# Kernel tuning notes

Hardware: AMD Instinct MI355X
Metric: run time of the kernel (lower is better)

Reference implementation:

```python
import jax, jax.numpy as jnp
import numpy as np

B, R, A, S, F, N = 2, 1, 16, 14, 1024, 512  # batch, num_rx, num_rx_ant, ofdm_symbols, fft_size, num_effective_sc
D = S * N  # flattened time-frequency dim that C acts on


def setup_inputs() -> dict:
    key = jax.random.key(0)
    k0, k1, k2, k3 = jax.random.split(key, 4)
    scale = 1.0 / np.sqrt(D).astype(np.float32)
    x_re = jax.random.normal(k0, (B, R, A, S, F), jnp.float32)
    x_im = jax.random.normal(k1, (B, R, A, S, F), jnp.float32)
    C_re = jax.random.normal(k2, (D, D), jnp.float32) * scale
    C_im = jax.random.normal(k3, (D, D), jnp.float32) * scale
    # unique, sorted effective-subcarrier indices (as in an OFDM ResourceGrid)
    sc_ind = jnp.asarray(np.sort(np.random.default_rng(0).choice(F, N, replace=False)), jnp.int32)
    return {"x_re": x_re, "x_im": x_im, "C_re": C_re, "C_im": C_im, "sc_ind": sc_ind}


def reference(x_re, x_im, C_re, C_im, sc_ind):
    x = jax.lax.complex(x_re, x_im)            # [B,R,A,S,F] complex64
    C = jax.lax.complex(C_re, C_im)            # [D,D]
    y = jnp.take(x, sc_ind, axis=-1)           # gather effective subcarriers -> [B,R,A,S,N]
    b, r, a, s, n = y.shape
    yf = y.reshape(b, r, a, s * n)             # flatten_last_dims(y, 2)
    # multiply_from_right with adjoint: yf @ C^H
    yf = jnp.einsum('brad,ed->brae', yf, jnp.conj(C))
    y = yf.reshape(b, r, a, s, n)
    # scatter back into full fft_size grid (unique indices -> set == scatter_nd on zeros)
    out = jnp.zeros((b, r, a, s, F), y.dtype).at[..., sc_ind].set(y)
    return jnp.stack([out.real, out.imag])     # [2,B,R,A,S,F] (real, imag)
```

## Files before the change

kernel.cpp:

```cpp
#include <hip/hip_runtime.h>
#include <hip/hip_bf16.h>

#define B_ 2
#define R_ 1
#define A_ 16
#define S_ 14
#define F_ 1024
#define N_ 512
#define D_ (S_*N_)
#define M_ (B_*R_*A_)
#define KK_ (2*D_)
#define BE 64
#define ETILES (D_/BE)

typedef __attribute__((ext_vector_type(8))) short bf16x8;
typedef __attribute__((ext_vector_type(4))) float f32x4;

static __device__ inline short f2bf(float f) {
    __hip_bfloat16 h = __float2bfloat16(f);
    return *reinterpret_cast<short*>(&h);
}
static __device__ inline float bf2f(short s) {
    unsigned int u = ((unsigned int)(unsigned short)s) << 16;
    return __uint_as_float(u);
}

#define LDSP(p) ((__attribute__((address_space(3))) void*)(p))
#define GLBP(p) ((const __attribute__((address_space(1))) void*)(p))

__global__ void prep_kernel(const float* __restrict__ xr, const float* __restrict__ xi,
                            const int* __restrict__ sc, short* __restrict__ Ap) {
    int idx = blockIdx.x * blockDim.x + threadIdx.x;
    if (idx >= 64 * KK_) return;
    int k = idx % KK_;
    int r = idx / KK_;
    int m = r & 31;
    int half = (k >= D_) ? 1 : 0;
    int d = half ? (k - D_) : k;
    int s = d >> 9;
    int n = d & 511;
    int f = sc[n];
    const float* base = (r < 32) ? (half ? xi : xr) : (half ? xr : xi);
    float v = base[(m * S_ + s) * F_ + f];
    if (r >= 32 && half) v = -v;
    Ap[idx] = f2bf(v);
}

__global__ void zero_kernel(float4* __restrict__ out, int n4) {
    int i = blockIdx.x * blockDim.x + threadIdx.x;
    if (i < n4) out[i] = make_float4(0.f, 0.f, 0.f, 0.f);
}

template<int KSPLIT, int PARTIALS>
__global__ __launch_bounds__(256) void gemm_kernel(
    const short* __restrict__ Ap,
    const float* __restrict__ Cre, const float* __restrict__ Cim,
    const int* __restrict__ sc,
    void* __restrict__ outp)
{
    constexpr int KBLK = KK_ / KSPLIT;
    constexpr int NCH  = KBLK / 32;
    __shared__ float Bl[2][64 * 32];
    __shared__ short Al[2][64 * 32];

    const int etile = blockIdx.x;
    const int ks    = blockIdx.y;
    const int tid   = threadIdx.x;
    const int wave  = tid >> 6;
    const int lane  = tid & 63;
    const int l16   = lane & 15;
    const int kg    = lane >> 4;

    const float* Cp = (ks < KSPLIT / 2) ? Cre : Cim;
    const int kc = (ks % (KSPLIT / 2)) * KBLK;
    const int ka = ks * KBLK;

    const float* bsrc[2];
    #pragma unroll
    for (int q = 0; q < 2; ++q) {
        int U = q * 256 + tid;
        int row = U >> 3;
        int u = (U & 7) ^ (row & 7);
        int p = u >> 1, h = u & 1;
        bsrc[q] = Cp + (size_t)(etile * 64 + row) * D_ + kc + p * 8 + h * 4;
    }
    const short* asrc = Ap + (size_t)(tid >> 2) * KK_ + ka + (tid & 3) * 8;

    {
        #pragma unroll
        for (int q = 0; q < 2; ++q)
            __builtin_amdgcn_global_load_lds(GLBP(bsrc[q]), LDSP(&Bl[0][(q * 256 + tid) * 4]), 16, 0, 0);
        __builtin_amdgcn_global_load_lds(GLBP(asrc), LDSP(&Al[0][tid * 8]), 16, 0, 0);
    }
    __syncthreads();

    f32x4 acc0 = {0.f,0.f,0.f,0.f}, acc1 = {0.f,0.f,0.f,0.f};
    f32x4 acc2 = {0.f,0.f,0.f,0.f}, acc3 = {0.f,0.f,0.f,0.f};

    const int row = wave * 16 + l16;
    const int swz = row & 7;
    const int boff = row * 32;
    const int u0 = ((kg * 2 + 0) ^ swz) * 4;
    const int u1 = ((kg * 2 + 1) ^ swz) * 4;

    for (int c = 0; c < NCH; ++c) {
        const int cur = c & 1;
        const int nxt = cur ^ 1;
        if (c + 1 < NCH) {
            #pragma unroll
            for (int q = 0; q < 2; ++q)
                __builtin_amdgcn_global_load_lds(GLBP(bsrc[q] + (c + 1) * 32),
                                                 LDSP(&Bl[nxt][(q * 256 + tid) * 4]), 16, 0, 0);
            __builtin_amdgcn_global_load_lds(GLBP(asrc + (c + 1) * 32),
                                             LDSP(&Al[nxt][tid * 8]), 16, 0, 0);
        }
        f32x4 b0 = *reinterpret_cast<const f32x4*>(&Bl[cur][boff + u0]);
        f32x4 b1 = *reinterpret_cast<const f32x4*>(&Bl[cur][boff + u1]);
        bf16x8 bf;
        bf[0] = f2bf(b0.x); bf[1] = f2bf(b0.y); bf[2] = f2bf(b0.z); bf[3] = f2bf(b0.w);
        bf[4] = f2bf(b1.x); bf[5] = f2bf(b1.y); bf[6] = f2bf(b1.z); bf[7] = f2bf(b1.w);
        bf16x8 a0 = *reinterpret_cast<const bf16x8*>(&Al[cur][(0 * 16 + l16) * 32 + kg * 8]);
        bf16x8 a1 = *reinterpret_cast<const bf16x8*>(&Al[cur][(1 * 16 + l16) * 32 + kg * 8]);
        bf16x8 a2 = *reinterpret_cast<const bf16x8*>(&Al[cur][(2 * 16 + l16) * 32 + kg * 8]);
        bf16x8 a3 = *reinterpret_cast<const bf16x8*>(&Al[cur][(3 * 16 + l16) * 32 + kg * 8]);
        acc0 = __builtin_amdgcn_mfma_f32_16x16x32_bf16(a0, bf, acc0, 0, 0, 0);
        acc1 = __builtin_amdgcn_mfma_f32_16x16x32_bf16(a1, bf, acc1, 0, 0, 0);
        acc2 = __builtin_amdgcn_mfma_f32_16x16x32_bf16(a2, bf, acc2, 0, 0, 0);
        acc3 = __builtin_amdgcn_mfma_f32_16x16x32_bf16(a3, bf, acc3, 0, 0, 0);
        __syncthreads();
    }

    const int e_lane = etile * 64 + row;
    if (PARTIALS) {
        short* part = (short*)outp + (size_t)ks * (64 * D_);
        #pragma unroll
        for (int mt = 0; mt < 4; ++mt) {
            f32x4 a = (mt == 0) ? acc0 : (mt == 1) ? acc1 : (mt == 2) ? acc2 : acc3;
            int rbase = mt * 16 + kg * 4;
            #pragma unroll
            for (int r = 0; r < 4; ++r)
                part[(size_t)(rbase + r) * D_ + e_lane] = f2bf(a[r]);
        }
    } else {
        float* out = (float*)outp;
        int s = e_lane >> 9, n = e_lane & 511;
        int f = sc[n];
        #pragma unroll
        for (int mt = 0; mt < 4; ++mt) {
            f32x4 a = (mt == 0) ? acc0 : (mt == 1) ? acc1 : (mt == 2) ? acc2 : acc3;
            int rbase = mt * 16 + kg * 4;
            #pragma unroll
            for (int r = 0; r < 4; ++r) {
                int rr = rbase + r;
                int pp = rr >> 5, m = rr & 31;
                atomicAdd(&out[((pp * M_ + m) * S_ + s) * F_ + f], a[r]);
            }
        }
    }
}

template<int KSPLIT>
__global__ void reduce_kernel(const short* __restrict__ part, const int* __restrict__ sc,
                              float* __restrict__ out) {
    int t = blockIdx.x * blockDim.x + threadIdx.x;
    if (t >= 64 * D_ / 8) return;
    int base = t * 8;
    int e0 = base % D_;
    int r  = base / D_;
    float v[8] = {0.f,0.f,0.f,0.f,0.f,0.f,0.f,0.f};
    #pragma unroll
    for (int ksp = 0; ksp < KSPLIT; ++ksp) {
        bf16x8 x = *reinterpret_cast<const bf16x8*>(&part[(size_t)ksp * (64 * D_) + base]);
        #pragma unroll
        for (int j = 0; j < 8; ++j) v[j] += bf2f(x[j]);
    }
    int pp = r >> 5, m = r & 31, s = e0 >> 9, n0 = e0 & 511;
    float* ob = &out[((pp * M_ + m) * S_ + s) * F_];
    #pragma unroll
    for (int j = 0; j < 8; ++j) ob[sc[n0 + j]] = v[j];
}

extern "C" void kernel_launch(void* const* d_in, const int* in_sizes, int n_in,
                              void* d_out, int out_size, void* d_ws, size_t ws_size,
                              hipStream_t stream) {
    const float* xr  = (const float*)d_in[0];
    const float* xi  = (const float*)d_in[1];
    const float* Cre = (const float*)d_in[2];
    const float* Cim = (const float*)d_in[3];
    const int*   sc  = (const int*)d_in[4];
    float* out = (float*)d_out;

    short* Ap = (short*)d_ws;
    const size_t partOff = 2u * 1024u * 1024u;
    const size_t need28  = partOff + 28ull * 64 * D_ * 2;
    const size_t need16  = partOff + 16ull * 64 * D_ * 2;

    prep_kernel<<<dim3((64 * KK_ + 255) / 256), 256, 0, stream>>>(xr, xi, sc, Ap);
    zero_kernel<<<dim3((917504 / 4 + 255) / 256), 256, 0, stream>>>((float4*)out, 917504 / 4);

    const int rthreads = 64 * D_ / 8;
    if (ws_size >= need28) {
        short* part = (short*)((char*)d_ws + partOff);
        gemm_kernel<28, 1><<<dim3(ETILES, 28), 256, 0, stream>>>(Ap, Cre, Cim, sc, part);
        reduce_kernel<28><<<dim3((rthreads + 255) / 256), 256, 0, stream>>>(part, sc, out);
    } else if (ws_size >= need16) {
        short* part = (short*)((char*)d_ws + partOff);
        gemm_kernel<16, 1><<<dim3(ETILES, 16), 256, 0, stream>>>(Ap, Cre, Cim, sc, part);
        reduce_kernel<16><<<dim3((rthreads + 255) / 256), 256, 0, stream>>>(part, sc, out);
    } else {
        gemm_kernel<16, 0><<<dim3(ETILES, 16), 256, 0, stream>>>(Ap, Cre, Cim, sc, out);
    }
}
```

Measured before the change: 116.2 us.

## Replace LDS-staged double buffering with direct global-to-register prefetch in GEMM

The GEMM kernel no longer stages C and A tiles through shared memory with global_load_lds and per-chunk barriers. Each lane now loads its C row fragment and A fragments straight from global memory into registers, using a two-deep register ping-pong to prefetch the next K chunk while the current one runs through MFMA. This drops the LDS traffic and the __syncthreads on every chunk, but the four waves no longer share A loads (each wave fetches the same A data, relying on cache) and more registers are live.

```diff
diff --git a/kernel.cpp b/kernel.cpp
--- a/kernel.cpp
+++ b/kernel.cpp
@@ -24,9 +24,6 @@
     unsigned int u = ((unsigned int)(unsigned short)s) << 16;
     return __uint_as_float(u);
 }
-
-#define LDSP(p) ((__attribute__((address_space(3))) void*)(p))
-#define GLBP(p) ((const __attribute__((address_space(1))) void*)(p))
 
 __global__ void prep_kernel(const float* __restrict__ xr, const float* __restrict__ xi,
                             const int* __restrict__ sc, short* __restrict__ Ap) {
@@ -59,10 +56,6 @@
     void* __restrict__ outp)
 {
     constexpr int KBLK = KK_ / KSPLIT;
-    constexpr int NCH  = KBLK / 32;
-    __shared__ float Bl[2][64 * 32];
-    __shared__ short Al[2][64 * 32];
-
     const int etile = blockIdx.x;
     const int ks    = blockIdx.y;
     const int tid   = threadIdx.x;
@@ -71,66 +64,58 @@
     const int l16   = lane & 15;
     const int kg    = lane >> 4;
 
-    const float* Cp = (ks < KSPLIT / 2) ? Cre : Cim;
+    const int e_lane = etile * BE + wave * 16 + l16;
+    const float* Cp  = (ks < KSPLIT / 2) ? Cre : Cim;
     const int kc = (ks % (KSPLIT / 2)) * KBLK;
     const int ka = ks * KBLK;
 
-    const float* bsrc[2];
-    #pragma unroll
-    for (int q = 0; q < 2; ++q) {
-        int U = q * 256 + tid;
-        int row = U >> 3;
-        int u = (U & 7) ^ (row & 7);
-        int p = u >> 1, h = u & 1;
-        bsrc[q] = Cp + (size_t)(etile * 64 + row) * D_ + kc + p * 8 + h * 4;
-    }
-    const short* asrc = Ap + (size_t)(tid >> 2) * KK_ + ka + (tid & 3) * 8;
+    const float* crow = Cp + (size_t)e_lane * D_ + kc + kg * 8;
+    const short* ab   = Ap + (size_t)l16 * KK_ + ka + kg * 8;
 
-    {
-        #pragma unroll
-        for (int q = 0; q < 2; ++q)
-            __builtin_amdgcn_global_load_lds(GLBP(bsrc[q]), LDSP(&Bl[0][(q * 256 + tid) * 4]), 16, 0, 0);
-        __builtin_amdgcn_global_load_lds(GLBP(asrc), LDSP(&Al[0][tid * 8]), 16, 0, 0);
-    }
-    __syncthreads();
+#define LB(b0, b1, off) do { \
+        b0 = *reinterpret_cast<const f32x4*>(crow + (off)); \
+        b1 = *reinterpret_cast<const f32x4*>(crow + (off) + 4); } while (0)
+#define LA(a0, a1, a2, a3, off) do { \
+        a0 = *reinterpret_cast<const bf16x8*>(ab + (off)); \
+        a1 = *reinterpret_cast<const bf16x8*>(ab + (size_t)16 * KK_ + (off)); \
+        a2 = *reinterpret_cast<const bf16x8*>(ab + (size_t)32 * KK_ + (off)); \
+        a3 = *reinterpret_cast<const bf16x8*>(ab + (size_t)48 * KK_ + (off)); } while (0)
+#define CMP(b0, b1, a0, a1, a2, a3) do { \
+        bf16x8 bf; \
+        bf[0] = f2bf(b0.x); bf[1] = f2bf(b0.y); bf[2] = f2bf(b0.z); bf[3] = f2bf(b0.w); \
+        bf[4] = f2bf(b1.x); bf[5] = f2bf(b1.y); bf[6] = f2bf(b1.z); bf[7] = f2bf(b1.w); \
+        acc0 = __builtin_amdgcn_mfma_f32_16x16x32_bf16(a0, bf, acc0, 0, 0, 0); \
+        acc1 = __builtin_amdgcn_mfma_f32_16x16x32_bf16(a1, bf, acc1, 0, 0, 0); \
+        acc2 = __builtin_amdgcn_mfma_f32_16x16x32_bf16(a2, bf, acc2, 0, 0, 0); \
+        acc3 = __builtin_amdgcn_mfma_f32_16x16x32_bf16(a3, bf, acc3, 0, 0, 0); } while (0)
 
     f32x4 acc0 = {0.f,0.f,0.f,0.f}, acc1 = {0.f,0.f,0.f,0.f};
     f32x4 acc2 = {0.f,0.f,0.f,0.f}, acc3 = {0.f,0.f,0.f,0.f};
 
-    const int row = wave * 16 + l16;
-    const int swz = row & 7;
-    const int boff = row * 32;
-    const int u0 = ((kg * 2 + 0) ^ swz) * 4;
-    const int u1 = ((kg * 2 + 1) ^ swz) * 4;
+    f32x4 pb0, pb1, qb0, qb1;
+    bf16x8 pa0, pa1, pa2, pa3, qa0, qa1, qa2, qa3;
 
-    for (int c = 0; c < NCH; ++c) {
-        const int cur = c & 1;
-        const int nxt = cur ^ 1;
-        if (c + 1 < NCH) {
-            #pragma unroll
-            for (int q = 0; q < 2; ++q)
-                __builtin_amdgcn_global_load_lds(GLBP(bsrc[q] + (c + 1) * 32),
-                                                 LDSP(&Bl[nxt][(q * 256 + tid) * 4]), 16, 0, 0);
-            __builtin_amdgcn_global_load_lds(GLBP(asrc + (c + 1) * 32),
-                                             LDSP(&Al[nxt][tid * 8]), 16, 0, 0);
-        }
-        f32x4 b0 = *reinterpret_cast<const f32x4*>(&Bl[cur][boff + u0]);
-        f32x4 b1 = *reinterpret_cast<const f32x4*>(&Bl[cur][boff + u1]);
-        bf16x8 bf;
-        bf[0] = f2bf(b0.x); bf[1] = f2bf(b0.y); bf[2] = f2bf(b0.z); bf[3] = f2bf(b0.w);
-        bf[4] = f2bf(b1.x); bf[5] = f2bf(b1.y); bf[6] = f2bf(b1.z); bf[7] = f2bf(b1.w);
-        bf16x8 a0 = *reinterpret_cast<const bf16x8*>(&Al[cur][(0 * 16 + l16) * 32 + kg * 8]);
-        bf16x8 a1 = *reinterpret_cast<const bf16x8*>(&Al[cur][(1 * 16 + l16) * 32 + kg * 8]);
-        bf16x8 a2 = *reinterpret_cast<const bf16x8*>(&Al[cur][(2 * 16 + l16) * 32 + kg * 8]);
-        bf16x8 a3 = *reinterpret_cast<const bf16x8*>(&Al[cur][(3 * 16 + l16) * 32 + kg * 8]);
-        acc0 = __builtin_amdgcn_mfma_f32_16x16x32_bf16(a0, bf, acc0, 0, 0, 0);
-        acc1 = __builtin_amdgcn_mfma_f32_16x16x32_bf16(a1, bf, acc1, 0, 0, 0);
-        acc2 = __builtin_amdgcn_mfma_f32_16x16x32_bf16(a2, bf, acc2, 0, 0, 0);
-        acc3 = __builtin_amdgcn_mfma_f32_16x16x32_bf16(a3, bf, acc3, 0, 0, 0);
-        __syncthreads();
+    LB(pb0, pb1, 0);
+    LA(pa0, pa1, pa2, pa3, 0);
+
+    int kk = 0;
+    for (; kk < KBLK - 64; kk += 64) {
+        LB(qb0, qb1, kk + 32);
+        LA(qa0, qa1, qa2, qa3, kk + 32);
+        CMP(pb0, pb1, pa0, pa1, pa2, pa3);
+        LB(pb0, pb1, kk + 64);
+        LA(pa0, pa1, pa2, pa3, kk + 64);
+        CMP(qb0, qb1, qa0, qa1, qa2, qa3);
     }
+    LB(qb0, qb1, kk + 32);
+    LA(qa0, qa1, qa2, qa3, kk + 32);
+    CMP(pb0, pb1, pa0, pa1, pa2, pa3);
+    CMP(qb0, qb1, qa0, qa1, qa2, qa3);
 
-    const int e_lane = etile * 64 + row;
+#undef LB
+#undef LA
+#undef CMP
+
     if (PARTIALS) {
         short* part = (short*)outp + (size_t)ks * (64 * D_);
         #pragma unroll
```

Result: slower. 184.9 us (+59.1%).

## Triple-buffer GEMM LDS pipeline with explicit waitcnt and k-blocked A layout

Applied to the files above, without the earlier changes.

Moves the GEMM main loop from double to triple buffering, issuing loads two chunks ahead and using explicit vmcnt/lgkmcnt waits with raw barriers in place of __syncthreads. The prep kernel now writes A in a k-blocked [k/8][64][8] layout, so each stage's A tile is one contiguous 4 KB load and the LDS reads are conflict-free. The B source addressing is simplified to the equivalent u*4 offset. This is meant to hide global load latency better, at the cost of more LDS and hand-tuned wait counts that must stay exactly right for correctness.

```diff
diff --git a/kernel.cpp b/kernel.cpp
--- a/kernel.cpp
+++ b/kernel.cpp
@@ -43,7 +43,7 @@
     const float* base = (r < 32) ? (half ? xi : xr) : (half ? xr : xi);
     float v = base[(m * S_ + s) * F_ + f];
     if (r >= 32 && half) v = -v;
-    Ap[idx] = f2bf(v);
+    Ap[((size_t)(k >> 3) * 64 + r) * 8 + (k & 7)] = f2bf(v);
 }
 
 __global__ void zero_kernel(float4* __restrict__ out, int n4) {
@@ -60,8 +60,8 @@
 {
     constexpr int KBLK = KK_ / KSPLIT;
     constexpr int NCH  = KBLK / 32;
-    __shared__ float Bl[2][64 * 32];
-    __shared__ short Al[2][64 * 32];
+    __shared__ float Bl[3][64 * 32];
+    __shared__ short Al[3][64 * 32];
 
     const int etile = blockIdx.x;
     const int ks    = blockIdx.y;
@@ -81,56 +81,62 @@
         int U = q * 256 + tid;
         int row = U >> 3;
         int u = (U & 7) ^ (row & 7);
-        int p = u >> 1, h = u & 1;
-        bsrc[q] = Cp + (size_t)(etile * 64 + row) * D_ + kc + p * 8 + h * 4;
-    }
-    const short* asrc = Ap + (size_t)(tid >> 2) * KK_ + ka + (tid & 3) * 8;
-
-    {
-        #pragma unroll
-        for (int q = 0; q < 2; ++q)
-            __builtin_amdgcn_global_load_lds(GLBP(bsrc[q]), LDSP(&Bl[0][(q * 256 + tid) * 4]), 16, 0, 0);
-        __builtin_amdgcn_global_load_lds(GLBP(asrc), LDSP(&Al[0][tid * 8]), 16, 0, 0);
-    }
-    __syncthreads();
+        bsrc[q] = Cp + (size_t)(etile * BE + row) * D_ + kc + u * 4;
+    }
+    const short* asrc = Ap + ((size_t)(ka >> 3) * 64) * 8 + tid * 8;
+
+#define STAGE(c) do { \
+        int bf_ = (c) % 3; \
+        __builtin_amdgcn_global_load_lds(GLBP(bsrc[0] + (size_t)(c) * 32), \
+                                         LDSP(&Bl[bf_][(0 * 256 + tid) * 4]), 16, 0, 0); \
+        __builtin_amdgcn_global_load_lds(GLBP(bsrc[1] + (size_t)(c) * 32), \
+                                         LDSP(&Bl[bf_][(1 * 256 + tid) * 4]), 16, 0, 0); \
+        __builtin_amdgcn_global_load_lds(GLBP(asrc + (size_t)(c) * 2048), \
+                                         LDSP(&Al[bf_][tid * 8]), 16, 0, 0); \
+    } while (0)
+
+    STAGE(0);
+    STAGE(1);
 
     f32x4 acc0 = {0.f,0.f,0.f,0.f}, acc1 = {0.f,0.f,0.f,0.f};
     f32x4 acc2 = {0.f,0.f,0.f,0.f}, acc3 = {0.f,0.f,0.f,0.f};
 
-    const int row = wave * 16 + l16;
-    const int swz = row & 7;
+    const int row  = wave * 16 + l16;
+    const int swz  = row & 7;
     const int boff = row * 32;
     const int u0 = ((kg * 2 + 0) ^ swz) * 4;
     const int u1 = ((kg * 2 + 1) ^ swz) * 4;
 
     for (int c = 0; c < NCH; ++c) {
-        const int cur = c & 1;
-        const int nxt = cur ^ 1;
-        if (c + 1 < NCH) {
-            #pragma unroll
-            for (int q = 0; q < 2; ++q)
-                __builtin_amdgcn_global_load_lds(GLBP(bsrc[q] + (c + 1) * 32),
-                                                 LDSP(&Bl[nxt][(q * 256 + tid) * 4]), 16, 0, 0);
-            __builtin_amdgcn_global_load_lds(GLBP(asrc + (c + 1) * 32),
-                                             LDSP(&Al[nxt][tid * 8]), 16, 0, 0);
-        }
-        f32x4 b0 = *reinterpret_cast<const f32x4*>(&Bl[cur][boff + u0]);
-        f32x4 b1 = *reinterpret_cast<const f32x4*>(&Bl[cur][boff + u1]);
-        bf16x8 bf;
-        bf[0] = f2bf(b0.x); bf[1] = f2bf(b0.y); bf[2] = f2bf(b0.z); bf[3] = f2bf(b0.w);
-        bf[4] = f2bf(b1.x); bf[5] = f2bf(b1.y); bf[6] = f2bf(b1.z); bf[7] = f2bf(b1.w);
-        bf16x8 a0 = *reinterpret_cast<const bf16x8*>(&Al[cur][(0 * 16 + l16) * 32 + kg * 8]);
-        bf16x8 a1 = *reinterpret_cast<const bf16x8*>(&Al[cur][(1 * 16 + l16) * 32 + kg * 8]);
-        bf16x8 a2 = *reinterpret_cast<const bf16x8*>(&Al[cur][(2 * 16 + l16) * 32 + kg * 8]);
-        bf16x8 a3 = *reinterpret_cast<const bf16x8*>(&Al[cur][(3 * 16 + l16) * 32 + kg * 8]);
-        acc0 = __builtin_amdgcn_mfma_f32_16x16x32_bf16(a0, bf, acc0, 0, 0, 0);
-        acc1 = __builtin_amdgcn_mfma_f32_16x16x32_bf16(a1, bf, acc1, 0, 0, 0);
-        acc2 = __builtin_amdgcn_mfma_f32_16x16x32_bf16(a2, bf, acc2, 0, 0, 0);
-        acc3 = __builtin_amdgcn_mfma_f32_16x16x32_bf16(a3, bf, acc3, 0, 0, 0);
-        __syncthreads();
-    }
-
-    const int e_lane = etile * 64 + row;
+        if (c < NCH - 1) asm volatile("s_waitcnt vmcnt(3)" ::: "memory");
+        else             asm volatile("s_waitcnt vmcnt(0)" ::: "memory");
+        __builtin_amdgcn_sched_barrier(0);
+        __builtin_amdgcn_s_barrier();
+
+        const int buf = c % 3;
+        f32x4 b0 = *reinterpret_cast<const f32x4*>(&Bl[buf][boff + u0]);
+        f32x4 b1 = *reinterpret_cast<const f32x4*>(&Bl[buf][boff + u1]);
+        bf16x8 a0 = *reinterpret_cast<const bf16x8*>(&Al[buf][(kg * 64 + 0 * 16 + l16) * 8]);
+        bf16x8 a1 = *reinterpret_cast<const bf16x8*>(&Al[buf][(kg * 64 + 1 * 16 + l16) * 8]);
+        bf16x8 a2 = *reinterpret_cast<const bf16x8*>(&Al[buf][(kg * 64 + 2 * 16 + l16) * 8]);
+        bf16x8 a3 = *reinterpret_cast<const bf16x8*>(&Al[buf][(kg * 64 + 3 * 16 + l16) * 8]);
+        asm volatile("s_waitcnt lgkmcnt(0)" ::: "memory");
+        __builtin_amdgcn_sched_barrier(0);
+        __builtin_amdgcn_s_barrier();
+
+        if (c + 2 < NCH) STAGE(c + 2);
+
+        bf16x8 bfv;
+        bfv[0] = f2bf(b0.x); bfv[1] = f2bf(b0.y); bfv[2] = f2bf(b0.z); bfv[3] = f2bf(b0.w);
+        bfv[4] = f2bf(b1.x); bfv[5] = f2bf(b1.y); bfv[6] = f2bf(b1.z); bfv[7] = f2bf(b1.w);
+        acc0 = __builtin_amdgcn_mfma_f32_16x16x32_bf16(a0, bfv, acc0, 0, 0, 0);
+        acc1 = __builtin_amdgcn_mfma_f32_16x16x32_bf16(a1, bfv, acc1, 0, 0, 0);
+        acc2 = __builtin_amdgcn_mfma_f32_16x16x32_bf16(a2, bfv, acc2, 0, 0, 0);
+        acc3 = __builtin_amdgcn_mfma_f32_16x16x32_bf16(a3, bfv, acc3, 0, 0, 0);
+    }
+#undef STAGE
+
+    const int e_lane = etile * BE + row;
     if (PARTIALS) {
         short* part = (short*)outp + (size_t)ks * (64 * D_);
         #pragma unroll
```

New measurement: 107.7 us. 7.3% less time.
